# Performance work log

Measured on AMD Instinct MI355X. Metric: run time of the kernel, lower is better.

The kernel has to match this reference:

```python
import jax, jax.numpy as jnp
import numpy as np

R, C = 30, 56
N = R * C  # 1680
K = 0.005
PRCN = 15
ALPHA = 1.0
BETA = 1.0


def setup_inputs() -> dict:
    key = jax.random.key(0)
    k1, k2 = jax.random.split(key)
    net_in = jax.random.normal(k1, (2 * N,), dtype=jnp.float32)
    # Recurrent connectivity matrix (learned weight in the original, loaded from .mat)
    J = jax.random.normal(k2, (N, N), dtype=jnp.float32) / np.float32(np.sqrt(N))
    return {"net_in": net_in, "J": J}


def reference(net_in, J):
    Iext = net_in[:N].reshape(R, C)
    r0 = net_in[N:2 * N].reshape(R, C)

    def step(r, _):
        # 4-way chunked mm + cat in the original == single matvec J @ r_flat
        temp = (J @ r.reshape(N)).reshape(R, C)
        U = ALPHA * (BETA * temp) + ALPHA * Iext
        sq = jnp.square(0.2 * U)
        recSum = jnp.sum(K * sq)
        # (0.2*U)^2 * (0.04 / recSum) / 0.04  ==  sq / recSum, kept explicit for fidelity
        r_new = sq * (0.04 / recSum) / 0.04
        return r_new, (U, recSum)

    r_last, (Us, sums) = jax.lax.scan(step, r0, None, length=PRCN - 1)
    return Us[-1], sums[-1], r_last
```

## Files before the change

kernel.cpp:

```cpp
#include <hip/hip_runtime.h>


#define N 1680
#define NV4 420
#define NBLK 420
#define NSTEP 14

__global__ __launch_bounds__(256) void step_kernel(
    const float* __restrict__ J,
    const float* __restrict__ net_in,
    const float* __restrict__ r_prev,
    float* __restrict__ r_new,
    const float* __restrict__ partials_prev,
    float* __restrict__ partials_cur,
    float* __restrict__ d_out,
    int first, int last)
{
    __shared__ float r_lds[N];
    __shared__ float sred[4];
    __shared__ float wsq[4];

    const int tid  = threadIdx.x;
    const int lane = tid & 63;
    const int wave = tid >> 6;

    const float4* rp4 = (const float4*)r_prev;
    float4* rl4 = (float4*)r_lds;
    for (int i = tid; i < NV4; i += 256) rl4[i] = rp4[i];

    float p = 0.0f;
    if (!first) {
        for (int i = tid; i < NBLK; i += 256) p += partials_prev[i];
    }
    #pragma unroll
    for (int off = 32; off; off >>= 1) p += __shfl_xor(p, off, 64);
    if (lane == 0) sred[wave] = p;
    __syncthreads();
    const float s_prev = first ? 1.0f : (sred[0] + sred[1] + sred[2] + sred[3]);

    const int row = blockIdx.x * 4 + wave;
    const float4* Jrow = (const float4*)(J + (size_t)row * N);
    float acc = 0.0f;
    #pragma unroll
    for (int k = 0; k < 7; ++k) {
        const int idx = lane + 64 * k;
        if (idx < NV4) {
            const float4 a = Jrow[idx];
            const float4 b = rl4[idx];
            acc += a.x * b.x + a.y * b.y + a.z * b.z + a.w * b.w;
        }
    }
    #pragma unroll
    for (int off = 32; off; off >>= 1) acc += __shfl_xor(acc, off, 64);

    if (lane == 0) {
        const float U  = acc / s_prev + net_in[row];
        const float u2 = 0.2f * U;
        const float sq = u2 * u2;
        r_new[row] = sq;
        if (last) d_out[row] = U;
        wsq[wave] = 0.005f * sq;
    }
    __syncthreads();
    if (tid == 0) partials_cur[blockIdx.x] = wsq[0] + wsq[1] + wsq[2] + wsq[3];
}

__global__ __launch_bounds__(256) void finish_kernel(
    const float* __restrict__ r_last_un,
    const float* __restrict__ partials_last,
    float* __restrict__ d_out)
{
    __shared__ float sred[4];
    const int tid  = threadIdx.x;
    const int lane = tid & 63;
    const int wave = tid >> 6;

    float p = 0.0f;
    for (int i = tid; i < NBLK; i += 256) p += partials_last[i];
    #pragma unroll
    for (int off = 32; off; off >>= 1) p += __shfl_xor(p, off, 64);
    if (lane == 0) sred[wave] = p;
    __syncthreads();
    const float s = sred[0] + sred[1] + sred[2] + sred[3];

    const int gid = blockIdx.x * 256 + tid;
    if (gid == 0) d_out[N] = s;
    if (gid < N) d_out[N + 1 + gid] = r_last_un[gid] / s;
}

extern "C" void kernel_launch(void* const* d_in, const int* in_sizes, int n_in,
                              void* d_out, int out_size, void* d_ws, size_t ws_size,
                              hipStream_t stream) {
    const float* net_in = (const float*)d_in[0];
    const float* J      = (const float*)d_in[1];
    float* out = (float*)d_out;
    float* ws  = (float*)d_ws;

    float* rbuf[2] = { ws, ws + 1792 };
    float* partials = ws + 3584;

    const float* r_prev = net_in + N;
    for (int t = 0; t < NSTEP; ++t) {
        float* r_new = rbuf[t & 1];
        const float* pp = (t == 0) ? nullptr : partials + (size_t)(t - 1) * NBLK;
        float* pc = partials + (size_t)t * NBLK;
        step_kernel<<<NBLK, 256, 0, stream>>>(J, net_in, r_prev, r_new, pp, pc,
                                              out, t == 0 ? 1 : 0, t == NSTEP - 1 ? 1 : 0);
        r_prev = r_new;
    }
    finish_kernel<<<7, 256, 0, stream>>>(r_prev, partials + (size_t)(NSTEP - 1) * NBLK, out);
}
```

Before: 120.7 us.

## Fuse all recurrence steps into one persistent kernel with grid-wide atomic barriers

Replaces the 14 per-step kernel launches plus a finish kernel with a single persistent kernel of 105 blocks. Each block keeps its 16 rows of J resident in registers across all steps and synchronises with the other blocks through per-step atomic counters in workspace. This removes repeated launch overhead and the repeated reads of J from memory each step. It risks deadlock if not all 105 blocks are co-resident, adds spin-wait latency, and needs a memset of the counters before every launch.

```diff
diff --git a/kernel.cpp b/kernel.cpp
--- a/kernel.cpp
+++ b/kernel.cpp
@@ -1,91 +1,154 @@
 #include <hip/hip_runtime.h>
 
 
-#define N 1680
-#define NV4 420
-#define NBLK 420
-#define NSTEP 14
+#define N      1680
+#define NV4    420
+#define NSTEP  14
+#define GBLK   105
+#define RPB    16
+#define RPW    4
 
-__global__ __launch_bounds__(256) void step_kernel(
+__global__ __launch_bounds__(256, 1) void fused_recur(
     const float* __restrict__ J,
     const float* __restrict__ net_in,
-    const float* __restrict__ r_prev,
-    float* __restrict__ r_new,
-    const float* __restrict__ partials_prev,
-    float* __restrict__ partials_cur,
-    float* __restrict__ d_out,
-    int first, int last)
+    float* __restrict__ out,
+    float* __restrict__ ws)
 {
     __shared__ float r_lds[N];
     __shared__ float sred[4];
     __shared__ float wsq[4];
 
+    unsigned* cnt = (unsigned*)ws;
+    float* rbuf0    = ws + 16;
+    float* rbuf1    = ws + 16 + 1792;
+    float* partials = ws + 16 + 2 * 1792;
+
     const int tid  = threadIdx.x;
     const int lane = tid & 63;
     const int wave = tid >> 6;
+    const int row0 = blockIdx.x * RPB + wave * RPW;
 
-    const float4* rp4 = (const float4*)r_prev;
+    float4 Jr[RPW][7];
+    #pragma unroll
+    for (int m = 0; m < RPW; ++m) {
+        const float4* Jrow = (const float4*)(J + (size_t)(row0 + m) * N);
+        #pragma unroll
+        for (int k = 0; k < 7; ++k) {
+            const int idx = lane + 64 * k;
+            Jr[m][k] = (idx < NV4) ? Jrow[idx] : make_float4(0.f, 0.f, 0.f, 0.f);
+        }
+    }
+    float iext[RPW];
+    #pragma unroll
+    for (int m = 0; m < RPW; ++m) iext[m] = net_in[row0 + m];
+
+    float Uv[RPW], Qv[RPW];
     float4* rl4 = (float4*)r_lds;
-    for (int i = tid; i < NV4; i += 256) rl4[i] = rp4[i];
 
+    for (int t = 0; t < NSTEP; ++t) {
+        float s_prev;
+        if (t == 0) {
+            const float4* rs4 = (const float4*)(net_in + N);
+            for (int i = tid; i < NV4; i += 256) rl4[i] = rs4[i];
+            __syncthreads();
+            s_prev = 1.0f;
+        } else {
+            if (tid == 0) {
+                while (__hip_atomic_load(&cnt[t - 1], __ATOMIC_RELAXED,
+                                         __HIP_MEMORY_SCOPE_AGENT) < GBLK)
+                    __builtin_amdgcn_s_sleep(1);
+            }
+            __syncthreads();
+            __threadfence();
+
+            const float* rsrc = (t & 1) ? rbuf0 : rbuf1;
+            const float4* rs4 = (const float4*)rsrc;
+            for (int i = tid; i < NV4; i += 256) rl4[i] = rs4[i];
+
+            float p = 0.0f;
+            if (tid < GBLK) p = partials[(t - 1) * GBLK + tid];
+            #pragma unroll
+            for (int off = 32; off; off >>= 1) p += __shfl_xor(p, off, 64);
+            if (lane == 0) sred[wave] = p;
+            __syncthreads();
+            s_prev = sred[0] + sred[1] + sred[2] + sred[3];
+        }
+
+        float4 rv[7];
+        #pragma unroll
+        for (int k = 0; k < 7; ++k) {
+            const int idx = lane + 64 * k;
+            rv[k] = (idx < NV4) ? rl4[idx] : make_float4(0.f, 0.f, 0.f, 0.f);
+        }
+
+        float a[RPW];
+        #pragma unroll
+        for (int m = 0; m < RPW; ++m) {
+            float acc = 0.0f;
+            #pragma unroll
+            for (int k = 0; k < 7; ++k) {
+                acc += Jr[m][k].x * rv[k].x;
+                acc += Jr[m][k].y * rv[k].y;
+                acc += Jr[m][k].z * rv[k].z;
+                acc += Jr[m][k].w * rv[k].w;
+            }
+            a[m] = acc;
+        }
+        #pragma unroll
+        for (int off = 32; off; off >>= 1) {
+            #pragma unroll
+            for (int m = 0; m < RPW; ++m) a[m] += __shfl_xor(a[m], off, 64);
+        }
+
+        float psum = 0.0f;
+        #pragma unroll
+        for (int m = 0; m < RPW; ++m) {
+            const float U  = a[m] / s_prev + iext[m];
+            const float u2 = 0.2f * U;
+            const float sq = u2 * u2;
+            Uv[m] = U;
+            Qv[m] = sq;
+            psum += sq;
+        }
+
+        if (lane == 0) {
+            wsq[wave] = 0.005f * psum;
+            if (t < NSTEP - 1) {
+                float* wb = (t & 1) ? rbuf1 : rbuf0;
+                *(float4*)(wb + row0) = make_float4(Qv[0], Qv[1], Qv[2], Qv[3]);
+            }
+        }
+        __syncthreads();
+        if (tid == 0) {
+            partials[t * GBLK + blockIdx.x] = wsq[0] + wsq[1] + wsq[2] + wsq[3];
+            __hip_atomic_fetch_add(&cnt[t], 1u, __ATOMIC_RELEASE,
+                                   __HIP_MEMORY_SCOPE_AGENT);
+        }
+    }
+
+    if (tid == 0) {
+        while (__hip_atomic_load(&cnt[NSTEP - 1], __ATOMIC_RELAXED,
+                                 __HIP_MEMORY_SCOPE_AGENT) < GBLK)
+            __builtin_amdgcn_s_sleep(1);
+    }
+    __syncthreads();
+    __threadfence();
     float p = 0.0f;
-    if (!first) {
-        for (int i = tid; i < NBLK; i += 256) p += partials_prev[i];
-    }
+    if (tid < GBLK) p = partials[(NSTEP - 1) * GBLK + tid];
     #pragma unroll
     for (int off = 32; off; off >>= 1) p += __shfl_xor(p, off, 64);
     if (lane == 0) sred[wave] = p;
     __syncthreads();
-    const float s_prev = first ? 1.0f : (sred[0] + sred[1] + sred[2] + sred[3]);
+    const float s13 = sred[0] + sred[1] + sred[2] + sred[3];
 
-    const int row = blockIdx.x * 4 + wave;
-    const float4* Jrow = (const float4*)(J + (size_t)row * N);
-    float acc = 0.0f;
-    #pragma unroll
-    for (int k = 0; k < 7; ++k) {
-        const int idx = lane + 64 * k;
-        if (idx < NV4) {
-            const float4 a = Jrow[idx];
-            const float4 b = rl4[idx];
-            acc += a.x * b.x + a.y * b.y + a.z * b.z + a.w * b.w;
-        }
+    if (lane == 0)
+        *(float4*)(out + row0) = make_float4(Uv[0], Uv[1], Uv[2], Uv[3]);
+    if (lane < RPW) {
+        const float q = (lane == 0) ? Qv[0] : (lane == 1) ? Qv[1]
+                       : (lane == 2) ? Qv[2] : Qv[3];
+        out[N + 1 + row0 + lane] = q / s13;
     }
-    #pragma unroll
-    for (int off = 32; off; off >>= 1) acc += __shfl_xor(acc, off, 64);
-
-    if (lane == 0) {
-        const float U  = acc / s_prev + net_in[row];
-        const float u2 = 0.2f * U;
-        const float sq = u2 * u2;
-        r_new[row] = sq;
-        if (last) d_out[row] = U;
-        wsq[wave] = 0.005f * sq;
-    }
-    __syncthreads();
-    if (tid == 0) partials_cur[blockIdx.x] = wsq[0] + wsq[1] + wsq[2] + wsq[3];
-}
-
-__global__ __launch_bounds__(256) void finish_kernel(
-    const float* __restrict__ r_last_un,
-    const float* __restrict__ partials_last,
-    float* __restrict__ d_out)
-{
-    __shared__ float sred[4];
-    const int tid  = threadIdx.x;
-    const int lane = tid & 63;
-    const int wave = tid >> 6;
-
-    float p = 0.0f;
-    for (int i = tid; i < NBLK; i += 256) p += partials_last[i];
-    #pragma unroll
-    for (int off = 32; off; off >>= 1) p += __shfl_xor(p, off, 64);
-    if (lane == 0) sred[wave] = p;
-    __syncthreads();
-    const float s = sred[0] + sred[1] + sred[2] + sred[3];
-
-    const int gid = blockIdx.x * 256 + tid;
-    if (gid == 0) d_out[N] = s;
-    if (gid < N) d_out[N + 1 + gid] = r_last_un[gid] / s;
+    if (blockIdx.x == 0 && tid == 0) out[N] = s13;
 }
 
 extern "C" void kernel_launch(void* const* d_in, const int* in_sizes, int n_in,
@@ -93,20 +156,6 @@
                               hipStream_t stream) {
     const float* net_in = (const float*)d_in[0];
     const float* J      = (const float*)d_in[1];
-    float* out = (float*)d_out;
-    float* ws  = (float*)d_ws;
-
-    float* rbuf[2] = { ws, ws + 1792 };
-    float* partials = ws + 3584;
-
-    const float* r_prev = net_in + N;
-    for (int t = 0; t < NSTEP; ++t) {
-        float* r_new = rbuf[t & 1];
-        const float* pp = (t == 0) ? nullptr : partials + (size_t)(t - 1) * NBLK;
-        float* pc = partials + (size_t)t * NBLK;
-        step_kernel<<<NBLK, 256, 0, stream>>>(J, net_in, r_prev, r_new, pp, pc,
-                                              out, t == 0 ? 1 : 0, t == NSTEP - 1 ? 1 : 0);
-        r_prev = r_new;
-    }
-    finish_kernel<<<7, 256, 0, stream>>>(r_prev, partials + (size_t)(NSTEP - 1) * NBLK, out);
+    hipMemsetAsync(d_ws, 0, 64, stream);
+    fused_recur<<<GBLK, 256, 0, stream>>>(J, net_in, (float*)d_out, (float*)d_ws);
 }
```

After: 224.0 us. +85.6%, slower.
